# Performance work log

Measured on AMD Instinct MI355X. Metric: run time of the kernel, lower is better.

The kernel has to match this reference:

```python
import jax, jax.numpy as jnp
import numpy as np

N = 262144   # flattened seq_len * num_agents
D = 256      # d_model
H = 256      # expert_hidden_dim
E = 4        # num_experts
C = 10       # num_classes
K = 2        # top-k


def setup_inputs() -> dict:
    key = jax.random.key(0)
    ks = jax.random.split(key, 8)
    def w(k, shape, fan_in):
        return jax.random.normal(k, shape, dtype=jnp.float32) / np.sqrt(fan_in).astype(np.float32)
    return {
        "x":   jax.random.normal(ks[0], (N, D), dtype=jnp.float32),
        # gate: Linear(D,D) -> GELU -> Linear(D,E)
        "Wg1": w(ks[1], (D, D), D), "bg1": jnp.zeros((D,), jnp.float32),
        "Wg2": w(ks[2], (D, E), D), "bg2": jnp.zeros((E,), jnp.float32),
        # experts (stacked): Linear(D,H) -> GELU -> Linear(H,C)
        "We1": w(ks[3], (E, D, H), D), "be1": jnp.zeros((E, H), jnp.float32),
        "We2": w(ks[4], (E, H, C), H), "be2": jnp.zeros((E, C), jnp.float32),
        # alpha head: Linear(D,H) -> GELU -> Linear(H,C) -> Softplus
        "Wa1": w(ks[5], (D, H), D), "ba1": jnp.zeros((H,), jnp.float32),
        "Wa2": w(ks[6], (H, C), H), "ba2": jnp.zeros((C,), jnp.float32),
    }


def reference(x, Wg1, bg1, Wg2, bg2, We1, be1, We2, be2, Wa1, ba1, Wa2, ba2):
    gelu = lambda v: jax.nn.gelu(v, approximate=False)  # torch nn.GELU default (erf)

    # --- noisy top-k gating (eval mode: no noise, no dropout) ---
    gate_logits = gelu(x @ Wg1 + bg1) @ Wg2 + bg2                      # [N, E]
    top_vals, top_idx = jax.lax.top_k(gate_logits, K)                  # [N, K]
    rows = jnp.arange(x.shape[0])[:, None]
    gw = jnp.zeros_like(gate_logits).at[rows, top_idx].set(top_vals)   # scatter top-k vals, zeros elsewhere
    gate_weights = jax.nn.softmax(gw, axis=-1)                         # softmax over ALL E slots (zeros included)
    load = gate_weights.sum(axis=0)                                    # [E]

    # --- dense expert ensemble ---
    h = gelu(jnp.einsum('nd,edh->neh', x, We1) + be1)                  # [N, E, H]
    expert_out = jnp.einsum('neh,ehc->nec', h, We2) + be2              # [N, E, C]
    logits = jnp.einsum('nec,ne->nc', expert_out, gate_weights)        # [N, C]

    # --- Dirichlet alpha head ---
    alpha = jax.nn.softplus(gelu(x @ Wa1 + ba1) @ Wa2 + ba2) + 1e-6    # [N, C]

    return logits, alpha, gate_weights, load
```

## Files before the change

kernel.cpp:

```cpp
#include <hip/hip_runtime.h>
#include <hip/hip_bf16.h>


typedef _Float16 f16x8 __attribute__((ext_vector_type(8)));
typedef _Float16 f16x4 __attribute__((ext_vector_type(4)));
typedef float    f32x4 __attribute__((ext_vector_type(4)));

static constexpr int    NTOK      = 262144;
static constexpr size_t ALPHA_OFF = (size_t)NTOK * 10;
static constexpr size_t GW_OFF    = (size_t)2 * NTOK * 10;
static constexpr size_t LOAD_OFF  = GW_OFF + (size_t)NTOK * 4;

static constexpr size_t W1F_OFF   = 0;
static constexpr size_t W2F_OFF   = 786432;
static constexpr size_t CNT_OFF   = 835584;
static constexpr size_t LIST_OFF  = 835648;
static constexpr size_t LPART_OFF = 1884224;

static constexpr float DELTA = 0.02f;

__device__ __forceinline__ float gelu_exact(float v){
  return 0.5f * v * (1.0f + erff(v * 0.7071067811865475f));
}
__device__ __forceinline__ float gelu_fast(float v){
  float t = v * v;
  float p = __builtin_fmaf(0.0713548162726f, t, 1.5957691216057f);
  float z = __expf(v * p);
  float r = __builtin_amdgcn_rcpf(z + 1.0f);
  return v - v * r;
}
__device__ __forceinline__ float softplus_fast(float v){
  float z = __expf(v);
  float l = __logf(1.0f + z);
  return (v > 15.0f) ? v : l;
}
__device__ __forceinline__ f32x4 mfma16(f16x8 a, f16x8 b, f32x4 c){
  return __builtin_amdgcn_mfma_f32_16x16x32_f16(a, b, c, 0, 0, 0);
}
__device__ __forceinline__ f16x8 pk8(float4 a, float4 b){
  union { f16x8 v; unsigned u[4]; } r;
  r.u[0] = __builtin_bit_cast(unsigned, __builtin_amdgcn_cvt_pkrtz(a.x, a.y));
  r.u[1] = __builtin_bit_cast(unsigned, __builtin_amdgcn_cvt_pkrtz(a.z, a.w));
  r.u[2] = __builtin_bit_cast(unsigned, __builtin_amdgcn_cvt_pkrtz(b.x, b.y));
  r.u[3] = __builtin_bit_cast(unsigned, __builtin_amdgcn_cvt_pkrtz(b.z, b.w));
  return r.v;
}
__device__ __forceinline__ f16x4 pk4(float a, float b, float c, float d){
  union { f16x4 v; unsigned u[2]; } r;
  r.u[0] = __builtin_bit_cast(unsigned, __builtin_amdgcn_cvt_pkrtz(a, b));
  r.u[1] = __builtin_bit_cast(unsigned, __builtin_amdgcn_cvt_pkrtz(c, d));
  return r.v;
}

__device__ __forceinline__ void topk4(float v0, float v1, float v2, float v3,
                                      float4& gw, float& gap, int& i1, int& i2){
  float m1 = fmaxf(fmaxf(v0, v1), fmaxf(v2, v3));
  i1 = (v0 == m1) ? 0 : (v1 == m1) ? 1 : (v2 == m1) ? 2 : 3;
  float m2 = 0.f; i2 = -1;
  if (0 != i1){ m2 = v0; i2 = 0; }
  if (1 != i1 && (i2 < 0 || v1 > m2)){ m2 = v1; i2 = 1; }
  if (2 != i1 && (i2 < 0 || v2 > m2)){ m2 = v2; i2 = 2; }
  if (3 != i1 && (i2 < 0 || v3 > m2)){ m2 = v3; i2 = 3; }
  float m3 = -3.0e38f;
  if (0 != i1 && 0 != i2) m3 = fmaxf(m3, v0);
  if (1 != i1 && 1 != i2) m3 = fmaxf(m3, v1);
  if (2 != i1 && 2 != i2) m3 = fmaxf(m3, v2);
  if (3 != i1 && 3 != i2) m3 = fmaxf(m3, v3);
  gap = m2 - m3;
  float mm = fmaxf(m1, 0.0f);
  float s0 = (0 == i1 || 0 == i2) ? v0 : 0.0f;
  float s1 = (1 == i1 || 1 == i2) ? v1 : 0.0f;
  float s2 = (2 == i1 || 2 == i2) ? v2 : 0.0f;
  float s3 = (3 == i1 || 3 == i2) ? v3 : 0.0f;
  float e0 = expf(s0 - mm), e1 = expf(s1 - mm), e2 = expf(s2 - mm), e3 = expf(s3 - mm);
  float inv = 1.0f / (e0 + e1 + e2 + e3);
  gw.x = e0 * inv; gw.y = e1 * inv; gw.z = e2 * inv; gw.w = e3 * inv;
}

__global__ void prep_w1f(const float* __restrict__ We1, const float* __restrict__ Wa1,
                         const float* __restrict__ Wg1, _Float16* __restrict__ W1F){
  int idx = blockIdx.x * 256 + threadIdx.x;
  int e = idx >> 13;
  int r = idx & 8191;
  int kc = r >> 10;
  int entry = r & 1023;
  int ht = entry >> 6, ll = entry & 63;
  int h = ht * 16 + (ll & 15);
  int d0 = kc * 32 + ((ll >> 4) << 3);
  f16x8 o;
  #pragma unroll
  for (int j = 0; j < 8; ++j){
    int d = d0 + j;
    float v;
    if (e < 4)       v = We1[e * 65536 + d * 256 + h];
    else if (e == 4) v = Wa1[d * 256 + h];
    else             v = Wg1[d * 256 + h];
    o[j] = (_Float16)v;
  }
  *(f16x8*)&W1F[(size_t)idx * 8] = o;
}

__global__ void prep_w2f(const float* __restrict__ We2, const float* __restrict__ Wa2,
                         const float* __restrict__ Wg2, _Float16* __restrict__ W2F,
                         unsigned int* __restrict__ cntp){
  if (blockIdx.x == 0 && threadIdx.x == 0) *cntp = 0;
  int idx = blockIdx.x * 256 + threadIdx.x;
  int e = idx >> 9;
  int r = idx & 511;
  int k2 = r >> 6, ll = r & 63;
  int c = ll & 15;
  int h0 = k2 * 32 + ((ll >> 4) << 3);
  f16x8 o;
  #pragma unroll
  for (int j = 0; j < 8; ++j){
    int h = h0 + j;
    float v = 0.0f;
    if (e < 4){ if (c < 10) v = We2[e * 2560 + h * 10 + c]; }
    else if (e == 4){ if (c < 10) v = Wa2[h * 10 + c]; }
    else { if (c < 4) v = Wg2[h * 4 + c]; }
    o[j] = (_Float16)v;
  }
  *(f16x8*)&W2F[(size_t)idx * 8] = o;
}

__device__ __forceinline__ void run_l1(const _Float16* __restrict__ w1s,
                                       const unsigned char* __restrict__ xsb,
                                       int w, int l, int l15, int lq,
                                       f32x4 acc[2][4]){
  #pragma unroll
  for (int kc = 0; kc < 8; ++kc){
    f16x8 af[2], bf[4];
    #pragma unroll
    for (int i = 0; i < 2; ++i)
      af[i] = *(const f16x8*)&w1s[(size_t)kc * 8192 + (w + 8 * i) * 512 + l * 8];
    #pragma unroll
    for (int tt = 0; tt < 4; ++tt){
      int lt = tt * 16 + l15;
      bf[tt] = *(const f16x8*)(xsb + lt * 512 +
                 ((kc * 64 + lq * 16) ^ ((lt & 15) << 4)));
    }
    __builtin_amdgcn_s_setprio(1);
    #pragma unroll
    for (int i = 0; i < 2; ++i)
      #pragma unroll
      for (int tt = 0; tt < 4; ++tt)
        acc[i][tt] = mfma16(af[i], bf[tt], acc[i][tt]);
    __builtin_amdgcn_s_setprio(0);
  }
}

__global__ __launch_bounds__(512, 4) void fused_kernel(
    const float* __restrict__ x,
    const _Float16* __restrict__ W1F, const _Float16* __restrict__ W2F,
    const float* __restrict__ bg1, const float* __restrict__ bg2,
    const float* __restrict__ be1, const float* __restrict__ be2,
    const float* __restrict__ ba1, const float* __restrict__ ba2,
    float* __restrict__ out, unsigned int* __restrict__ list,
    unsigned int* __restrict__ cntp, float* __restrict__ lpart){
  __shared__ __align__(16) unsigned char lds[49216];
  unsigned char* xsb = lds;
  unsigned char* hsb = lds + 32768;
  float*        lsum = (float*)(lds + 49152);

  const int tid = threadIdx.x;
  const int w = tid >> 6, l = tid & 63;
  const int l15 = l & 15, lq = l >> 4;
  const size_t t0 = (size_t)blockIdx.x * 64;
  const int tokL = (w & 3) * 16 + l15;
  const int key  = (tokL & 15) << 4;

  {
    int d = (tid & 31) * 8;
    #pragma unroll
    for (int q = 0; q < 4; ++q){
      int tk = q * 16 + (tid >> 5);
      const float* xp = x + (t0 + tk) * 256 + d;
      float4 f0 = *(const float4*)xp;
      float4 f1 = *(const float4*)(xp + 4);
      *(f16x8*)(xsb + tk * 512 + ((d * 2) ^ ((tk & 15) << 4))) = pk8(f0, f1);
    }
  }
  __syncthreads();

  f32x4 lacc = {0,0,0,0};
  float4 gw4 = {0,0,0,0};

  for (int s = 0; s < 6; ++s){
    const int e = (s == 0) ? 5 : (s - 1);
    f32x4 acc[2][4];
    #pragma unroll
    for (int i = 0; i < 2; ++i)
      #pragma unroll
      for (int tt = 0; tt < 4; ++tt){
        acc[i][tt][0]=0.f; acc[i][tt][1]=0.f; acc[i][tt][2]=0.f; acc[i][tt][3]=0.f;
      }
    run_l1(W1F + (size_t)e * 65536, xsb, w, l, l15, lq, acc);

    const float* b1p = (e == 5) ? bg1 : (e < 4 ? be1 + e * 256 : ba1);
    f32x4 d2 = {0,0,0,0};
    #pragma unroll
    for (int p = 0; p < 2; ++p){
      __syncthreads();
      {
        int hb = (w + 8 * p) * 16 + lq * 4;
        float4 b4 = *(const float4*)&b1p[hb];
        int lb = (w * 16 + lq * 4) * 2;
        #pragma unroll
        for (int tt = 0; tt < 4; ++tt){
          f16x4 hv = pk4(gelu_fast(acc[p][tt][0] + b4.x),
                         gelu_fast(acc[p][tt][1] + b4.y),
                         gelu_fast(acc[p][tt][2] + b4.z),
                         gelu_fast(acc[p][tt][3] + b4.w));
          int lt = tt * 16 + l15;
          *(f16x4*)(hsb + lt * 256 + (lb ^ ((lt & 15) << 4))) = hv;
        }
      }
      __syncthreads();
      #pragma unroll
      for (int k2h = 0; k2h < 4; ++k2h){
        int k2 = 4 * p + k2h;
        f16x8 a2 = *(const f16x8*)&W2F[((size_t)(e * 8 + k2) * 64 + l) * 8];
        f16x8 b2 = *(const f16x8*)(hsb + tokL * 256 + ((k2h * 64 + lq * 16) ^ key));
        d2 = mfma16(a2, b2, d2);
      }
    }

    if (s == 0){
      float4 gw = {0,0,0,0};
      float4 lgw = {0,0,0,0};
      int i1 = 0, i2 = 0;
      bool flagged = false;
      if (lq == 0){
        float v0 = d2[0] + bg2[0], v1 = d2[1] + bg2[1];
        float v2 = d2[2] + bg2[2], v3 = d2[3] + bg2[3];
        float gap;
        topk4(v0, v1, v2, v3, gw, gap, i1, i2);
        if (w < 4){
          size_t t = t0 + tokL;
          *(float4*)&out[GW_OFF + t * 4] = gw;
          flagged = (gap < DELTA);
          lgw = gw;
        }
      }
      gw4.x = __shfl(gw.x, l15, 64);
      gw4.y = __shfl(gw.y, l15, 64);
      gw4.z = __shfl(gw.z, l15, 64);
      gw4.w = __shfl(gw.w, l15, 64);
      if (w < 4){
        unsigned long long m = __ballot(flagged);
        int cnt = __popcll(m);
        if (cnt){
          unsigned base = 0;
          if (l == 0) base = atomicAdd(cntp, (unsigned)cnt);
          base = __shfl(base, 0, 64);
          if (flagged){
            unsigned rank = (unsigned)__popcll(m & ((1ull << l) - 1ull));
            list[base + rank] = (unsigned)(t0 + tokL) | (i1 << 18) | (i2 << 20);
          }
        }
        #pragma unroll
        for (int mm = 1; mm < 64; mm <<= 1){
          lgw.x += __shfl_xor(lgw.x, mm, 64); lgw.y += __shfl_xor(lgw.y, mm, 64);
          lgw.z += __shfl_xor(lgw.z, mm, 64); lgw.w += __shfl_xor(lgw.w, mm, 64);
        }
        if (l == 0) *(float4*)&lsum[w * 4] = lgw;
      }
      __syncthreads();
      if (tid < 4)
        lpart[(size_t)blockIdx.x * 4 + tid] =
            lsum[tid] + lsum[4 + tid] + lsum[8 + tid] + lsum[12 + tid];
    } else if (e < 4){
      float gwv = (e == 0) ? gw4.x : (e == 1) ? gw4.y : (e == 2) ? gw4.z : gw4.w;
      #pragma unroll
      for (int r = 0; r < 4; ++r){
        int c = lq * 4 + r;
        float bv = (c < 10) ? be2[e * 10 + c] : 0.0f;
        lacc[r] += gwv * (d2[r] + bv);
      }
    } else {
      if (w < 4){
        size_t t = t0 + tokL;
        #pragma unroll
        for (int r = 0; r < 4; ++r){
          int c = lq * 4 + r;
          if (c < 10)
            out[ALPHA_OFF + t * 10 + c] = softplus_fast(d2[r] + ba2[c]) + 1e-6f;
        }
      }
    }
  }
  if (w < 4){
    size_t t = t0 + tokL;
    #pragma unroll
    for (int r = 0; r < 4; ++r){
      int c = lq * 4 + r;
      if (c < 10) out[t * 10 + c] = lacc[r];
    }
  }
}

__global__ __launch_bounds__(256) void refine_kernel(
    const float* __restrict__ x, const float* __restrict__ Wg1,
    const float* __restrict__ bg1, const float* __restrict__ Wg2,
    const float* __restrict__ bg2,
    const float* __restrict__ We1, const float* __restrict__ be1,
    const float* __restrict__ We2, const float* __restrict__ be2,
    const unsigned int* __restrict__ list, const unsigned int* __restrict__ cntp,
    float* __restrict__ out){
  int cnt = (int)*cntp;
  int l = threadIdx.x & 63;
  int hb = l * 4;
  for (int idx = blockIdx.x * 4 + (threadIdx.x >> 6); idx < cnt;
       idx += gridDim.x * 4){
    unsigned ent = list[idx];
    int t = (int)(ent & 0x3FFFFu);
    int oi1 = (ent >> 18) & 3, oi2 = (ent >> 20) & 3;
    const float* xr = x + (size_t)t * 256;
    float a0 = 0.f, a1 = 0.f, a2 = 0.f, a3 = 0.f;
    #pragma unroll 8
    for (int d = 0; d < 256; ++d){
      float xv = xr[d];
      float4 wv = *(const float4*)&Wg1[d * 256 + hb];
      a0 = fmaf(xv, wv.x, a0); a1 = fmaf(xv, wv.y, a1);
      a2 = fmaf(xv, wv.z, a2); a3 = fmaf(xv, wv.w, a3);
    }
    float4 b4 = *(const float4*)&bg1[hb];
    float g0 = gelu_exact(a0 + b4.x), g1 = gelu_exact(a1 + b4.y);
    float g2 = gelu_exact(a2 + b4.z), g3 = gelu_exact(a3 + b4.w);
    float4 w0 = *(const float4*)&Wg2[(hb + 0) * 4];
    float4 w1 = *(const float4*)&Wg2[(hb + 1) * 4];
    float4 w2 = *(const float4*)&Wg2[(hb + 2) * 4];
    float4 w3 = *(const float4*)&Wg2[(hb + 3) * 4];
    float p0 = g0 * w0.x + g1 * w1.x + g2 * w2.x + g3 * w3.x;
    float p1 = g0 * w0.y + g1 * w1.y + g2 * w2.y + g3 * w3.y;
    float p2 = g0 * w0.z + g1 * w1.z + g2 * w2.z + g3 * w3.z;
    float p3 = g0 * w0.w + g1 * w1.w + g2 * w2.w + g3 * w3.w;
    #pragma unroll
    for (int m = 1; m < 64; m <<= 1){
      p0 += __shfl_xor(p0, m, 64); p1 += __shfl_xor(p1, m, 64);
      p2 += __shfl_xor(p2, m, 64); p3 += __shfl_xor(p3, m, 64);
    }
    float4 gw; float gap; int i1, i2;
    topk4(p0 + bg2[0], p1 + bg2[1], p2 + bg2[2], p3 + bg2[3], gw, gap, i1, i2);
    if (l == 0) *(float4*)&out[GW_OFF + (size_t)t * 4] = gw;
    int oldset = (1 << oi1) | (1 << oi2);
    int newset = (1 << i1) | (1 << i2);
    if (oldset != newset){
      float lg[10];
      #pragma unroll
      for (int c = 0; c < 10; ++c) lg[c] = 0.f;
      for (int e = 0; e < 4; ++e){
        float gwe = (e == 0) ? gw.x : (e == 1) ? gw.y : (e == 2) ? gw.z : gw.w;
        float c0 = 0.f, c1 = 0.f, c2 = 0.f, c3 = 0.f;
        #pragma unroll 8
        for (int d = 0; d < 256; ++d){
          float xv = xr[d];
          float4 wv = *(const float4*)&We1[e * 65536 + d * 256 + hb];
          c0 = fmaf(xv, wv.x, c0); c1 = fmaf(xv, wv.y, c1);
          c2 = fmaf(xv, wv.z, c2); c3 = fmaf(xv, wv.w, c3);
        }
        float4 be = *(const float4*)&be1[e * 256 + hb];
        float h[4];
        h[0] = gelu_exact(c0 + be.x); h[1] = gelu_exact(c1 + be.y);
        h[2] = gelu_exact(c2 + be.z); h[3] = gelu_exact(c3 + be.w);
        #pragma unroll
        for (int r = 0; r < 4; ++r){
          const float* w2p = &We2[e * 2560 + (hb + r) * 10];
          #pragma unroll
          for (int c = 0; c < 10; ++c) lg[c] += gwe * (h[r] * w2p[c]);
        }
      }
      #pragma unroll
      for (int m = 1; m < 64; m <<= 1)
        #pragma unroll
        for (int c = 0; c < 10; ++c) lg[c] += __shfl_xor(lg[c], m, 64);
      if (l == 0){
        #pragma unroll
        for (int c = 0; c < 10; ++c)
          out[(size_t)t * 10 + c] = lg[c] + gw.x * be2[c] + gw.y * be2[10 + c]
                                         + gw.z * be2[20 + c] + gw.w * be2[30 + c];
      }
    }
  }
}

__global__ void reduce_load(const float* __restrict__ lpart, float* __restrict__ out){
  __shared__ float red[4][4];
  int tid = threadIdx.x;
  const float4* lp = (const float4*)lpart;
  float4 v = {0,0,0,0};
  #pragma unroll
  for (int j = 0; j < 16; ++j){
    float4 t = lp[tid + 256 * j];
    v.x += t.x; v.y += t.y; v.z += t.z; v.w += t.w;
  }
  #pragma unroll
  for (int m = 1; m < 64; m <<= 1){
    v.x += __shfl_xor(v.x, m, 64); v.y += __shfl_xor(v.y, m, 64);
    v.z += __shfl_xor(v.z, m, 64); v.w += __shfl_xor(v.w, m, 64);
  }
  if ((tid & 63) == 0){
    red[tid >> 6][0] = v.x; red[tid >> 6][1] = v.y;
    red[tid >> 6][2] = v.z; red[tid >> 6][3] = v.w;
  }
  __syncthreads();
  if (tid < 4)
    out[LOAD_OFF + tid] = red[0][tid] + red[1][tid] + red[2][tid] + red[3][tid];
}

extern "C" void kernel_launch(void* const* d_in, const int* in_sizes, int n_in,
                              void* d_out, int out_size, void* d_ws, size_t ws_size,
                              hipStream_t stream){
  const float* x   = (const float*)d_in[0];
  const float* Wg1 = (const float*)d_in[1];
  const float* bg1 = (const float*)d_in[2];
  const float* Wg2 = (const float*)d_in[3];
  const float* bg2 = (const float*)d_in[4];
  const float* We1 = (const float*)d_in[5];
  const float* be1 = (const float*)d_in[6];
  const float* We2 = (const float*)d_in[7];
  const float* be2 = (const float*)d_in[8];
  const float* Wa1 = (const float*)d_in[9];
  const float* ba1 = (const float*)d_in[10];
  const float* Wa2 = (const float*)d_in[11];
  const float* ba2 = (const float*)d_in[12];
  float* out = (float*)d_out;

  _Float16* W1F       = (_Float16*)((char*)d_ws + W1F_OFF);
  _Float16* W2F       = (_Float16*)((char*)d_ws + W2F_OFF);
  unsigned int* cntp  = (unsigned int*)((char*)d_ws + CNT_OFF);
  unsigned int* list  = (unsigned int*)((char*)d_ws + LIST_OFF);
  float* lpart        = (float*)((char*)d_ws + LPART_OFF);

  hipLaunchKernelGGL(prep_w1f, dim3(192), dim3(256), 0, stream, We1, Wa1, Wg1, W1F);
  hipLaunchKernelGGL(prep_w2f, dim3(12),  dim3(256), 0, stream, We2, Wa2, Wg2, W2F, cntp);
  hipLaunchKernelGGL(fused_kernel, dim3(4096), dim3(512), 0, stream,
                     x, W1F, W2F, bg1, bg2, be1, be2, ba1, ba2,
                     out, list, cntp, lpart);
  hipLaunchKernelGGL(refine_kernel, dim3(1024), dim3(256), 0, stream,
                     x, Wg1, bg1, Wg2, bg2, We1, be1, We2, be2, list, cntp, out);
  hipLaunchKernelGGL(reduce_load, dim3(1), dim3(256), 0, stream, lpart, out);
}
```

Measured before the change: 557.2 us.

## Double-buffer hidden LDS tile and batch four tokens per wave in refine

The fused kernel now uses two separate LDS buffers for the two hidden halves, which removes one __syncthreads per pass. LDS per block grows from about 49KB to about 65KB. The refine kernel processes four flagged tokens per wave, so each Wg1 row load is reused across four tokens instead of one. That adds register pressure and padding work in the tail, and the larger LDS footprint may lower occupancy in the main kernel.

```diff
diff --git a/kernel.cpp b/kernel.cpp
--- a/kernel.cpp
+++ b/kernel.cpp
@@ -157,10 +157,11 @@
     const float* __restrict__ ba1, const float* __restrict__ ba2,
     float* __restrict__ out, unsigned int* __restrict__ list,
     unsigned int* __restrict__ cntp, float* __restrict__ lpart){
-  __shared__ __align__(16) unsigned char lds[49216];
+  __shared__ __align__(16) unsigned char lds[65600];
   unsigned char* xsb = lds;
-  unsigned char* hsb = lds + 32768;
-  float*        lsum = (float*)(lds + 49152);
+  unsigned char* hs0 = lds + 32768;
+  unsigned char* hs1 = lds + 49152;
+  float*        lsum = (float*)(lds + 65536);
 
   const int tid = threadIdx.x;
   const int w = tid >> 6, l = tid & 63;
@@ -200,7 +201,7 @@
     f32x4 d2 = {0,0,0,0};
     #pragma unroll
     for (int p = 0; p < 2; ++p){
-      __syncthreads();
+      unsigned char* hb_ = p ? hs1 : hs0;
       {
         int hb = (w + 8 * p) * 16 + lq * 4;
         float4 b4 = *(const float4*)&b1p[hb];
@@ -212,7 +213,7 @@
                          gelu_fast(acc[p][tt][2] + b4.z),
                          gelu_fast(acc[p][tt][3] + b4.w));
           int lt = tt * 16 + l15;
-          *(f16x4*)(hsb + lt * 256 + (lb ^ ((lt & 15) << 4))) = hv;
+          *(f16x4*)(hb_ + lt * 256 + (lb ^ ((lt & 15) << 4))) = hv;
         }
       }
       __syncthreads();
@@ -220,7 +221,7 @@
       for (int k2h = 0; k2h < 4; ++k2h){
         int k2 = 4 * p + k2h;
         f16x8 a2 = *(const f16x8*)&W2F[((size_t)(e * 8 + k2) * 64 + l) * 8];
-        f16x8 b2 = *(const f16x8*)(hsb + tokL * 256 + ((k2h * 64 + lq * 16) ^ key));
+        f16x8 b2 = *(const f16x8*)(hb_ + tokL * 256 + ((k2h * 64 + lq * 16) ^ key));
         d2 = mfma16(a2, b2, d2);
       }
     }
@@ -310,75 +311,90 @@
   int cnt = (int)*cntp;
   int l = threadIdx.x & 63;
   int hb = l * 4;
-  for (int idx = blockIdx.x * 4 + (threadIdx.x >> 6); idx < cnt;
-       idx += gridDim.x * 4){
-    unsigned ent = list[idx];
-    int t = (int)(ent & 0x3FFFFu);
-    int oi1 = (ent >> 18) & 3, oi2 = (ent >> 20) & 3;
-    const float* xr = x + (size_t)t * 256;
-    float a0 = 0.f, a1 = 0.f, a2 = 0.f, a3 = 0.f;
-    #pragma unroll 8
+  int wave = blockIdx.x * 4 + (threadIdx.x >> 6);
+  int stride4 = gridDim.x * 4 * 4;
+  for (int base = wave * 4; base < cnt; base += stride4){
+    unsigned ent[4]; int tk[4];
+    #pragma unroll
+    for (int k = 0; k < 4; ++k){
+      int ix = base + k; if (ix >= cnt) ix = cnt - 1;
+      ent[k] = list[ix];
+      tk[k] = (int)(ent[k] & 0x3FFFFu);
+    }
+    float a[4][4];
+    #pragma unroll
+    for (int k = 0; k < 4; ++k){ a[k][0]=0.f; a[k][1]=0.f; a[k][2]=0.f; a[k][3]=0.f; }
+    #pragma unroll 4
     for (int d = 0; d < 256; ++d){
-      float xv = xr[d];
       float4 wv = *(const float4*)&Wg1[d * 256 + hb];
-      a0 = fmaf(xv, wv.x, a0); a1 = fmaf(xv, wv.y, a1);
-      a2 = fmaf(xv, wv.z, a2); a3 = fmaf(xv, wv.w, a3);
+      #pragma unroll
+      for (int k = 0; k < 4; ++k){
+        float xv = x[(size_t)tk[k] * 256 + d];
+        a[k][0] = fmaf(xv, wv.x, a[k][0]); a[k][1] = fmaf(xv, wv.y, a[k][1]);
+        a[k][2] = fmaf(xv, wv.z, a[k][2]); a[k][3] = fmaf(xv, wv.w, a[k][3]);
+      }
     }
     float4 b4 = *(const float4*)&bg1[hb];
-    float g0 = gelu_exact(a0 + b4.x), g1 = gelu_exact(a1 + b4.y);
-    float g2 = gelu_exact(a2 + b4.z), g3 = gelu_exact(a3 + b4.w);
     float4 w0 = *(const float4*)&Wg2[(hb + 0) * 4];
     float4 w1 = *(const float4*)&Wg2[(hb + 1) * 4];
     float4 w2 = *(const float4*)&Wg2[(hb + 2) * 4];
     float4 w3 = *(const float4*)&Wg2[(hb + 3) * 4];
-    float p0 = g0 * w0.x + g1 * w1.x + g2 * w2.x + g3 * w3.x;
-    float p1 = g0 * w0.y + g1 * w1.y + g2 * w2.y + g3 * w3.y;
-    float p2 = g0 * w0.z + g1 * w1.z + g2 * w2.z + g3 * w3.z;
-    float p3 = g0 * w0.w + g1 * w1.w + g2 * w2.w + g3 * w3.w;
-    #pragma unroll
-    for (int m = 1; m < 64; m <<= 1){
-      p0 += __shfl_xor(p0, m, 64); p1 += __shfl_xor(p1, m, 64);
-      p2 += __shfl_xor(p2, m, 64); p3 += __shfl_xor(p3, m, 64);
-    }
-    float4 gw; float gap; int i1, i2;
-    topk4(p0 + bg2[0], p1 + bg2[1], p2 + bg2[2], p3 + bg2[3], gw, gap, i1, i2);
-    if (l == 0) *(float4*)&out[GW_OFF + (size_t)t * 4] = gw;
-    int oldset = (1 << oi1) | (1 << oi2);
-    int newset = (1 << i1) | (1 << i2);
-    if (oldset != newset){
-      float lg[10];
-      #pragma unroll
-      for (int c = 0; c < 10; ++c) lg[c] = 0.f;
-      for (int e = 0; e < 4; ++e){
-        float gwe = (e == 0) ? gw.x : (e == 1) ? gw.y : (e == 2) ? gw.z : gw.w;
-        float c0 = 0.f, c1 = 0.f, c2 = 0.f, c3 = 0.f;
-        #pragma unroll 8
-        for (int d = 0; d < 256; ++d){
-          float xv = xr[d];
-          float4 wv = *(const float4*)&We1[e * 65536 + d * 256 + hb];
-          c0 = fmaf(xv, wv.x, c0); c1 = fmaf(xv, wv.y, c1);
-          c2 = fmaf(xv, wv.z, c2); c3 = fmaf(xv, wv.w, c3);
-        }
-        float4 be = *(const float4*)&be1[e * 256 + hb];
-        float h[4];
-        h[0] = gelu_exact(c0 + be.x); h[1] = gelu_exact(c1 + be.y);
-        h[2] = gelu_exact(c2 + be.z); h[3] = gelu_exact(c3 + be.w);
+    #pragma unroll
+    for (int k = 0; k < 4; ++k){
+      if (base + k >= cnt) break;
+      int t = tk[k];
+      float g0 = gelu_exact(a[k][0] + b4.x), g1 = gelu_exact(a[k][1] + b4.y);
+      float g2 = gelu_exact(a[k][2] + b4.z), g3 = gelu_exact(a[k][3] + b4.w);
+      float p0 = g0 * w0.x + g1 * w1.x + g2 * w2.x + g3 * w3.x;
+      float p1 = g0 * w0.y + g1 * w1.y + g2 * w2.y + g3 * w3.y;
+      float p2 = g0 * w0.z + g1 * w1.z + g2 * w2.z + g3 * w3.z;
+      float p3 = g0 * w0.w + g1 * w1.w + g2 * w2.w + g3 * w3.w;
+      #pragma unroll
+      for (int m = 1; m < 64; m <<= 1){
+        p0 += __shfl_xor(p0, m, 64); p1 += __shfl_xor(p1, m, 64);
+        p2 += __shfl_xor(p2, m, 64); p3 += __shfl_xor(p3, m, 64);
+      }
+      float4 gw; float gap; int i1, i2;
+      topk4(p0 + bg2[0], p1 + bg2[1], p2 + bg2[2], p3 + bg2[3], gw, gap, i1, i2);
+      if (l == 0) *(float4*)&out[GW_OFF + (size_t)t * 4] = gw;
+      int oldset = (1 << ((ent[k] >> 18) & 3)) | (1 << ((ent[k] >> 20) & 3));
+      int newset = (1 << i1) | (1 << i2);
+      if (oldset != newset){
+        const float* xr = x + (size_t)t * 256;
+        float lg[10];
         #pragma unroll
-        for (int r = 0; r < 4; ++r){
-          const float* w2p = &We2[e * 2560 + (hb + r) * 10];
+        for (int c = 0; c < 10; ++c) lg[c] = 0.f;
+        for (int e = 0; e < 4; ++e){
+          float gwe = (e == 0) ? gw.x : (e == 1) ? gw.y : (e == 2) ? gw.z : gw.w;
+          float c0 = 0.f, c1 = 0.f, c2 = 0.f, c3 = 0.f;
+          #pragma unroll 8
+          for (int d = 0; d < 256; ++d){
+            float xv = xr[d];
+            float4 wv = *(const float4*)&We1[e * 65536 + d * 256 + hb];
+            c0 = fmaf(xv, wv.x, c0); c1 = fmaf(xv, wv.y, c1);
+            c2 = fmaf(xv, wv.z, c2); c3 = fmaf(xv, wv.w, c3);
+          }
+          float4 be = *(const float4*)&be1[e * 256 + hb];
+          float h[4];
+          h[0] = gelu_exact(c0 + be.x); h[1] = gelu_exact(c1 + be.y);
+          h[2] = gelu_exact(c2 + be.z); h[3] = gelu_exact(c3 + be.w);
           #pragma unroll
-          for (int c = 0; c < 10; ++c) lg[c] += gwe * (h[r] * w2p[c]);
-        }
-      }
-      #pragma unroll
-      for (int m = 1; m < 64; m <<= 1)
+          for (int r = 0; r < 4; ++r){
+            const float* w2p = &We2[e * 2560 + (hb + r) * 10];
+            #pragma unroll
+            for (int c = 0; c < 10; ++c) lg[c] += gwe * (h[r] * w2p[c]);
+          }
+        }
         #pragma unroll
-        for (int c = 0; c < 10; ++c) lg[c] += __shfl_xor(lg[c], m, 64);
-      if (l == 0){
-        #pragma unroll
-        for (int c = 0; c < 10; ++c)
-          out[(size_t)t * 10 + c] = lg[c] + gw.x * be2[c] + gw.y * be2[10 + c]
-                                         + gw.z * be2[20 + c] + gw.w * be2[30 + c];
+        for (int m = 1; m < 64; m <<= 1)
+          #pragma unroll
+          for (int c = 0; c < 10; ++c) lg[c] += __shfl_xor(lg[c], m, 64);
+        if (l == 0){
+          #pragma unroll
+          for (int c = 0; c < 10; ++c)
+            out[(size_t)t * 10 + c] = lg[c] + gw.x * be2[c] + gw.y * be2[10 + c]
+                                           + gw.z * be2[20 + c] + gw.w * be2[30 + c];
+        }
       }
     }
   }
```

After: 629.4 us. 1.13x slower.

## Pair two experts per layer-1 pass and double-buffer hidden LDS tiles

Applied to the files above, without the earlier changes.

The first-layer GEMM now processes two experts at once, so each x fragment read from LDS feeds four MFMAs instead of two. Passes drop from six to three. The hidden-activation buffer is split into two LDS halves, which removes one barrier per epilogue half, and the second-layer MFMAs now run only on the waves whose results are used. In exchange the kernel holds twice as many accumulator registers and uses more LDS. That may cause spills under the launch bounds or lower the number of resident blocks.

```diff
diff --git a/kernel.cpp b/kernel.cpp
--- a/kernel.cpp
+++ b/kernel.cpp
@@ -123,30 +123,40 @@
   *(f16x8*)&W2F[(size_t)idx * 8] = o;
 }
 
-__device__ __forceinline__ void run_l1(const _Float16* __restrict__ w1s,
-                                       const unsigned char* __restrict__ xsb,
-                                       int w, int l, int l15, int lq,
-                                       f32x4 acc[2][4]){
+__device__ __forceinline__ f32x4 epi_l2(const f32x4 (&accS)[2][4],
+    const float* __restrict__ b1p, const _Float16* __restrict__ W2F, int e,
+    unsigned char* hs0, unsigned char* hs1,
+    int w, int l, int l15, int lq, int tokL, int key){
+  f32x4 d2 = {0,0,0,0};
   #pragma unroll
-  for (int kc = 0; kc < 8; ++kc){
-    f16x8 af[2], bf[4];
-    #pragma unroll
-    for (int i = 0; i < 2; ++i)
-      af[i] = *(const f16x8*)&w1s[(size_t)kc * 8192 + (w + 8 * i) * 512 + l * 8];
-    #pragma unroll
-    for (int tt = 0; tt < 4; ++tt){
-      int lt = tt * 16 + l15;
-      bf[tt] = *(const f16x8*)(xsb + lt * 512 +
-                 ((kc * 64 + lq * 16) ^ ((lt & 15) << 4)));
-    }
-    __builtin_amdgcn_s_setprio(1);
-    #pragma unroll
-    for (int i = 0; i < 2; ++i)
-      #pragma unroll
-      for (int tt = 0; tt < 4; ++tt)
-        acc[i][tt] = mfma16(af[i], bf[tt], acc[i][tt]);
-    __builtin_amdgcn_s_setprio(0);
-  }
+  for (int p = 0; p < 2; ++p){
+    unsigned char* hb_ = p ? hs1 : hs0;
+    {
+      int hb = (w + 8 * p) * 16 + lq * 4;
+      float4 b4 = *(const float4*)&b1p[hb];
+      int lb = (w * 16 + lq * 4) * 2;
+      #pragma unroll
+      for (int tt = 0; tt < 4; ++tt){
+        f16x4 hv = pk4(gelu_fast(accS[p][tt][0] + b4.x),
+                       gelu_fast(accS[p][tt][1] + b4.y),
+                       gelu_fast(accS[p][tt][2] + b4.z),
+                       gelu_fast(accS[p][tt][3] + b4.w));
+        int lt = tt * 16 + l15;
+        *(f16x4*)(hb_ + lt * 256 + (lb ^ ((lt & 15) << 4))) = hv;
+      }
+    }
+    __syncthreads();
+    if (w < 4){
+      #pragma unroll
+      for (int k2h = 0; k2h < 4; ++k2h){
+        int k2 = 4 * p + k2h;
+        f16x8 a2 = *(const f16x8*)&W2F[((size_t)(e * 8 + k2) * 64 + l) * 8];
+        f16x8 b2 = *(const f16x8*)(hb_ + tokL * 256 + ((k2h * 64 + lq * 16) ^ key));
+        d2 = mfma16(a2, b2, d2);
+      }
+    }
+  }
+  return d2;
 }
 
 __global__ __launch_bounds__(512, 4) void fused_kernel(
@@ -157,10 +167,11 @@
     const float* __restrict__ ba1, const float* __restrict__ ba2,
     float* __restrict__ out, unsigned int* __restrict__ list,
     unsigned int* __restrict__ cntp, float* __restrict__ lpart){
-  __shared__ __align__(16) unsigned char lds[49216];
+  __shared__ __align__(16) unsigned char lds[65600];
   unsigned char* xsb = lds;
-  unsigned char* hsb = lds + 32768;
-  float*        lsum = (float*)(lds + 49152);
+  unsigned char* hs0 = lds + 32768;
+  unsigned char* hs1 = lds + 49152;
+  float*        lsum = (float*)(lds + 65536);
 
   const int tid = threadIdx.x;
   const int w = tid >> 6, l = tid & 63;
@@ -185,106 +196,117 @@
   f32x4 lacc = {0,0,0,0};
   float4 gw4 = {0,0,0,0};
 
-  for (int s = 0; s < 6; ++s){
-    const int e = (s == 0) ? 5 : (s - 1);
-    f32x4 acc[2][4];
+  #pragma unroll 1
+  for (int pr = 0; pr < 3; ++pr){
+    const int eA = (pr == 0) ? 5 : (pr == 1 ? 1 : 3);
+    const int eB = (pr == 0) ? 0 : (pr == 1 ? 2 : 4);
+    const _Float16* wAp = W1F + (size_t)eA * 65536;
+    const _Float16* wBp = W1F + (size_t)eB * 65536;
+
+    f32x4 accA[2][4], accB[2][4];
     #pragma unroll
     for (int i = 0; i < 2; ++i)
       #pragma unroll
       for (int tt = 0; tt < 4; ++tt){
-        acc[i][tt][0]=0.f; acc[i][tt][1]=0.f; acc[i][tt][2]=0.f; acc[i][tt][3]=0.f;
-      }
-    run_l1(W1F + (size_t)e * 65536, xsb, w, l, l15, lq, acc);
-
-    const float* b1p = (e == 5) ? bg1 : (e < 4 ? be1 + e * 256 : ba1);
-    f32x4 d2 = {0,0,0,0};
+        accA[i][tt][0]=0.f; accA[i][tt][1]=0.f; accA[i][tt][2]=0.f; accA[i][tt][3]=0.f;
+        accB[i][tt][0]=0.f; accB[i][tt][1]=0.f; accB[i][tt][2]=0.f; accB[i][tt][3]=0.f;
+      }
     #pragma unroll
-    for (int p = 0; p < 2; ++p){
-      __syncthreads();
-      {
-        int hb = (w + 8 * p) * 16 + lq * 4;
-        float4 b4 = *(const float4*)&b1p[hb];
-        int lb = (w * 16 + lq * 4) * 2;
-        #pragma unroll
-        for (int tt = 0; tt < 4; ++tt){
-          f16x4 hv = pk4(gelu_fast(acc[p][tt][0] + b4.x),
-                         gelu_fast(acc[p][tt][1] + b4.y),
-                         gelu_fast(acc[p][tt][2] + b4.z),
-                         gelu_fast(acc[p][tt][3] + b4.w));
-          int lt = tt * 16 + l15;
-          *(f16x4*)(hsb + lt * 256 + (lb ^ ((lt & 15) << 4))) = hv;
-        }
-      }
-      __syncthreads();
-      #pragma unroll
-      for (int k2h = 0; k2h < 4; ++k2h){
-        int k2 = 4 * p + k2h;
-        f16x8 a2 = *(const f16x8*)&W2F[((size_t)(e * 8 + k2) * 64 + l) * 8];
-        f16x8 b2 = *(const f16x8*)(hsb + tokL * 256 + ((k2h * 64 + lq * 16) ^ key));
-        d2 = mfma16(a2, b2, d2);
-      }
-    }
-
-    if (s == 0){
-      float4 gw = {0,0,0,0};
-      float4 lgw = {0,0,0,0};
-      int i1 = 0, i2 = 0;
-      bool flagged = false;
-      if (lq == 0){
-        float v0 = d2[0] + bg2[0], v1 = d2[1] + bg2[1];
-        float v2 = d2[2] + bg2[2], v3 = d2[3] + bg2[3];
-        float gap;
-        topk4(v0, v1, v2, v3, gw, gap, i1, i2);
-        if (w < 4){
+    for (int kc = 0; kc < 8; ++kc){
+      f16x8 afA0 = *(const f16x8*)&wAp[(size_t)kc * 8192 + (w    ) * 512 + l * 8];
+      f16x8 afA1 = *(const f16x8*)&wAp[(size_t)kc * 8192 + (w + 8) * 512 + l * 8];
+      f16x8 afB0 = *(const f16x8*)&wBp[(size_t)kc * 8192 + (w    ) * 512 + l * 8];
+      f16x8 afB1 = *(const f16x8*)&wBp[(size_t)kc * 8192 + (w + 8) * 512 + l * 8];
+      __builtin_amdgcn_s_setprio(1);
+      #pragma unroll
+      for (int tt = 0; tt < 4; ++tt){
+        int lt = tt * 16 + l15;
+        f16x8 bf = *(const f16x8*)(xsb + lt * 512 +
+                     ((kc * 64 + lq * 16) ^ ((lt & 15) << 4)));
+        accA[0][tt] = mfma16(afA0, bf, accA[0][tt]);
+        accA[1][tt] = mfma16(afA1, bf, accA[1][tt]);
+        accB[0][tt] = mfma16(afB0, bf, accB[0][tt]);
+        accB[1][tt] = mfma16(afB1, bf, accB[1][tt]);
+      }
+      __builtin_amdgcn_s_setprio(0);
+    }
+
+    {
+      const float* b1p = (eA == 5) ? bg1 : (be1 + eA * 256);
+      f32x4 d2 = epi_l2(accA, b1p, W2F, eA, hs0, hs1, w, l, l15, lq, tokL, key);
+      if (pr == 0){
+        float4 gw = {0,0,0,0};
+        float4 lgw = {0,0,0,0};
+        int i1 = 0, i2 = 0;
+        bool flagged = false;
+        if (lq == 0 && w < 4){
+          float v0 = d2[0] + bg2[0], v1 = d2[1] + bg2[1];
+          float v2 = d2[2] + bg2[2], v3 = d2[3] + bg2[3];
+          float gap;
+          topk4(v0, v1, v2, v3, gw, gap, i1, i2);
           size_t t = t0 + tokL;
           *(float4*)&out[GW_OFF + t * 4] = gw;
           flagged = (gap < DELTA);
           lgw = gw;
         }
-      }
-      gw4.x = __shfl(gw.x, l15, 64);
-      gw4.y = __shfl(gw.y, l15, 64);
-      gw4.z = __shfl(gw.z, l15, 64);
-      gw4.w = __shfl(gw.w, l15, 64);
-      if (w < 4){
-        unsigned long long m = __ballot(flagged);
-        int cnt = __popcll(m);
-        if (cnt){
-          unsigned base = 0;
-          if (l == 0) base = atomicAdd(cntp, (unsigned)cnt);
-          base = __shfl(base, 0, 64);
-          if (flagged){
-            unsigned rank = (unsigned)__popcll(m & ((1ull << l) - 1ull));
-            list[base + rank] = (unsigned)(t0 + tokL) | (i1 << 18) | (i2 << 20);
+        gw4.x = __shfl(gw.x, l15, 64);
+        gw4.y = __shfl(gw.y, l15, 64);
+        gw4.z = __shfl(gw.z, l15, 64);
+        gw4.w = __shfl(gw.w, l15, 64);
+        if (w < 4){
+          unsigned long long m = __ballot(flagged);
+          int cnt = __popcll(m);
+          if (cnt){
+            unsigned base = 0;
+            if (l == 0) base = atomicAdd(cntp, (unsigned)cnt);
+            base = __shfl(base, 0, 64);
+            if (flagged){
+              unsigned rank = (unsigned)__popcll(m & ((1ull << l) - 1ull));
+              list[base + rank] = (unsigned)(t0 + tokL) | (i1 << 18) | (i2 << 20);
+            }
           }
-        }
-        #pragma unroll
-        for (int mm = 1; mm < 64; mm <<= 1){
-          lgw.x += __shfl_xor(lgw.x, mm, 64); lgw.y += __shfl_xor(lgw.y, mm, 64);
-          lgw.z += __shfl_xor(lgw.z, mm, 64); lgw.w += __shfl_xor(lgw.w, mm, 64);
-        }
-        if (l == 0) *(float4*)&lsum[w * 4] = lgw;
-      }
-      __syncthreads();
-      if (tid < 4)
-        lpart[(size_t)blockIdx.x * 4 + tid] =
-            lsum[tid] + lsum[4 + tid] + lsum[8 + tid] + lsum[12 + tid];
-    } else if (e < 4){
-      float gwv = (e == 0) ? gw4.x : (e == 1) ? gw4.y : (e == 2) ? gw4.z : gw4.w;
-      #pragma unroll
-      for (int r = 0; r < 4; ++r){
-        int c = lq * 4 + r;
-        float bv = (c < 10) ? be2[e * 10 + c] : 0.0f;
-        lacc[r] += gwv * (d2[r] + bv);
-      }
-    } else {
-      if (w < 4){
-        size_t t = t0 + tokL;
+          #pragma unroll
+          for (int mm = 1; mm < 64; mm <<= 1){
+            lgw.x += __shfl_xor(lgw.x, mm, 64); lgw.y += __shfl_xor(lgw.y, mm, 64);
+            lgw.z += __shfl_xor(lgw.z, mm, 64); lgw.w += __shfl_xor(lgw.w, mm, 64);
+          }
+          if (l == 0) *(float4*)&lsum[w * 4] = lgw;
+        }
+        __syncthreads();
+        if (tid < 4)
+          lpart[(size_t)blockIdx.x * 4 + tid] =
+              lsum[tid] + lsum[4 + tid] + lsum[8 + tid] + lsum[12 + tid];
+      } else if (w < 4){
+        float gwv = (eA == 1) ? gw4.y : gw4.w;
         #pragma unroll
         for (int r = 0; r < 4; ++r){
           int c = lq * 4 + r;
-          if (c < 10)
-            out[ALPHA_OFF + t * 10 + c] = softplus_fast(d2[r] + ba2[c]) + 1e-6f;
+          float bv = (c < 10) ? be2[eA * 10 + c] : 0.0f;
+          lacc[r] += gwv * (d2[r] + bv);
+        }
+      }
+    }
+
+    {
+      const float* b1p = (eB == 4) ? ba1 : (be1 + eB * 256);
+      f32x4 d2 = epi_l2(accB, b1p, W2F, eB, hs0, hs1, w, l, l15, lq, tokL, key);
+      if (w < 4){
+        if (eB < 4){
+          float gwv = (eB == 0) ? gw4.x : gw4.z;
+          #pragma unroll
+          for (int r = 0; r < 4; ++r){
+            int c = lq * 4 + r;
+            float bv = (c < 10) ? be2[eB * 10 + c] : 0.0f;
+            lacc[r] += gwv * (d2[r] + bv);
+          }
+        } else {
+          size_t t = t0 + tokL;
+          #pragma unroll
+          for (int r = 0; r < 4; ++r){
+            int c = lq * 4 + r;
+            if (c < 10)
+              out[ALPHA_OFF + t * 10 + c] = softplus_fast(d2[r] + ba2[c]) + 1e-6f;
+          }
         }
       }
     }
```

Measured after the change: 677.2 us. 1.22x slower.
